# Kernel tuning notes

Hardware: AMD Instinct MI355X
Metric: run time of the kernel (lower is better)

The kernel has to match this reference:

```python
import jax, jax.numpy as jnp
import numpy as np

EMBED = 1024
HEADS = 16
HEAD_DIM = EMBED // HEADS
DIVIDER = int(np.sqrt(HEAD_DIM))  # torch code uses int(sqrt(head_dim)) == 8


def setup_inputs() -> dict:
    key = jax.random.key(0)
    ks = jax.random.split(key, 9)
    B, S = 2, 2048
    scale = 1.0 / np.sqrt(EMBED)
    def lin(kw, kb):
        W = jax.random.uniform(kw, (EMBED, EMBED), jnp.float32, -scale, scale)
        b = jax.random.uniform(kb, (EMBED,), jnp.float32, -scale, scale)
        return W, b
    Wq, bq = lin(ks[0], ks[1])
    Wk, bk = lin(ks[2], ks[3])
    Wv, bv = lin(ks[4], ks[5])
    Wo, bo = lin(ks[6], ks[7])
    x = jax.random.normal(ks[8], (B, S, EMBED), jnp.float32)
    return {"x": x, "Wq": Wq, "bq": bq, "Wk": Wk, "bk": bk,
            "Wv": Wv, "bv": bv, "Wo": Wo, "bo": bo}


def reference(x, Wq, bq, Wk, bk, Wv, bv, Wo, bo):
    B, S, _ = x.shape
    # projections (torch Linear: x @ W.T + b)
    q = x @ Wq.T + bq
    k = x @ Wk.T + bk
    v = x @ Wv.T + bv
    # split heads: [B, S, H, D] -> [B, H, S, D]
    def heads(t):
        return t.reshape(B, S, HEADS, HEAD_DIM).transpose(0, 2, 1, 3)
    q, k, v = heads(q), heads(k), heads(v)
    # scores [B, H, S, S]
    scores = jnp.einsum('bhsd,bhtd->bhst', q, k) / DIVIDER
    attn = jax.nn.softmax(scores, axis=-1)
    out = jnp.einsum('bhst,bhtd->bhsd', attn, v)
    out = out.transpose(0, 2, 1, 3).reshape(B, S, EMBED)
    return out @ Wo.T + bo
```

## Files before the change

kernel.cpp:

```cpp
#include <hip/hip_runtime.h>
#include <hip/hip_bf16.h>
#include <stdint.h>

using bf16 = __hip_bfloat16;
typedef __attribute__((ext_vector_type(8))) short   short8;
typedef __attribute__((ext_vector_type(4))) float   floatx4;
typedef __attribute__((ext_vector_type(2))) unsigned int uint2v;

static __device__ __forceinline__ unsigned short f2bf(float f) {
    return __builtin_bit_cast(unsigned short, __float2bfloat16(f));
}

static __device__ __forceinline__ uint4 load8bf(const void* p, size_t e, int f) {
    if (!f) return *(const uint4*)((const ushort*)p + e);
    const float* fp = (const float*)p + e;
    float4 a = *(const float4*)fp;
    float4 b = *(const float4*)(fp + 4);
    union { uint4 u; unsigned short s[8]; } r;
    r.s[0] = f2bf(a.x); r.s[1] = f2bf(a.y); r.s[2] = f2bf(a.z); r.s[3] = f2bf(a.w);
    r.s[4] = f2bf(b.x); r.s[5] = f2bf(b.y); r.s[6] = f2bf(b.z); r.s[7] = f2bf(b.w);
    return r.u;
}
static __device__ __forceinline__ float loadScalar(const void* p, int i, int f) {
    return f ? ((const float*)p)[i] : __bfloat162float(((const bf16*)p)[i]);
}

#define GLL16(g, l)                                                          \
    __builtin_amdgcn_global_load_lds(                                        \
        (const __attribute__((address_space(1))) void*)(g),                  \
        (__attribute__((address_space(3))) void*)(l), 16, 0, 0)

__global__ void detect_dtype(const ushort* __restrict__ x, int* __restrict__ flag) {
    __shared__ int cnt;
    if (threadIdx.x == 0) cnt = 0;
    __syncthreads();
    unsigned short u = x[threadIdx.x * 2];
    int e = (u >> 7) & 0xFF;
    int bad = (e > 133 || e < 94) ? 1 : 0;
    atomicAdd(&cnt, bad);
    __syncthreads();
    if (threadIdx.x == 0) *flag = (cnt > 64) ? 1 : 0;
}

__global__ void cvt_bf16(const void* __restrict__ x,  const void* __restrict__ Wq,
                         const void* __restrict__ Wk, const void* __restrict__ Wv,
                         const void* __restrict__ Wo,
                         ushort* __restrict__ out, const int* __restrict__ flagp)
{
    const int f = *flagp;
    const size_t M1 = (size_t)1 << 20, M4 = (size_t)4 << 20;
    size_t i = ((size_t)blockIdx.x * 256 + threadIdx.x) * 8;
    const void* src; size_t off;
    if (i < M4)            { src = x;  off = i; }
    else if (i < M4 + M1)  { src = Wq; off = i - M4; }
    else if (i < M4 + 2*M1){ src = Wk; off = i - (M4 + M1); }
    else if (i < M4 + 3*M1){ src = Wv; off = i - (M4 + 2*M1); }
    else                   { src = Wo; off = i - (M4 + 3*M1); }
    *(uint4*)(out + i) = load8bf(src, off, f);
}

__global__ __launch_bounds__(512, 4)
void gemm_lds(const ushort* __restrict__ A,
              const ushort* __restrict__ Wa, const ushort* __restrict__ Wb2,
              const void* __restrict__ Ba, const void* __restrict__ Bb,
              void* __restrict__ Oa, void* __restrict__ Ob_,
              int pa, int pb, int out_ext, const int* __restrict__ flagp)
{
    __shared__ ushort pool[24576];

    const int f  = *flagp;
    const int z  = blockIdx.z;
    const ushort* W  = z ? Wb2 : Wa;
    const void*  Bi  = z ? Bb : Ba;
    void*        Out = z ? Ob_ : Oa;
    const int    pm  = z ? pb : pa;

    const int m0 = blockIdx.x * 128;
    const int n0 = blockIdx.y * 64;
    const int tid  = threadIdx.x;
    const int lane = tid & 63;
    const int wave = tid >> 6;
    const int r15  = lane & 15;
    const int quad = lane >> 4;

    const int l8 = lane >> 3, s8 = lane & 7;
    const int ar0 = wave * 16 + l8;
    const int ar1 = wave * 16 + 8 + l8;
    const int wr  = wave * 8 + l8;
    const ushort* gA0 = A + (size_t)(m0 + ar0) * 1024 + ((s8 ^ (ar0 & 7)) << 3);
    const ushort* gA1 = A + (size_t)(m0 + ar1) * 1024 + ((s8 ^ (ar1 & 7)) << 3);
    const ushort* gW  = W + (size_t)(n0 + wr) * 1024 + ((s8 ^ (wr & 7)) << 3);

    floatx4 acc[4];
#pragma unroll
    for (int db = 0; db < 4; db++) acc[db] = (floatx4){0.f, 0.f, 0.f, 0.f};

    GLL16(gA0, pool + wave * 1024);
    GLL16(gA1, pool + wave * 1024 + 512);
    GLL16(gW,  pool + 16384 + wave * 512);

    for (int kb = 0; kb < 1024; kb += 64) {
        const int cur = (kb >> 6) & 1;
        ushort* xs  = pool + cur * 8192;
        ushort* wsm = pool + 16384 + cur * 4096;
        if (kb + 64 < 1024) {
            ushort* xn = pool + (cur ^ 1) * 8192;
            ushort* wn = pool + 16384 + (cur ^ 1) * 4096;
            GLL16(gA0 + kb + 64, xn + wave * 1024);
            GLL16(gA1 + kb + 64, xn + wave * 1024 + 512);
            GLL16(gW  + kb + 64, wn + wave * 512);
            asm volatile("s_waitcnt vmcnt(3)" ::: "memory");
        } else {
            asm volatile("s_waitcnt vmcnt(0)" ::: "memory");
        }
        __builtin_amdgcn_s_barrier();
        __builtin_amdgcn_sched_barrier(0);
#pragma unroll
        for (int ks = 0; ks < 2; ks++) {
            int arow = wave * 16 + r15;
            short8 af = *(const short8*)(
                &xs[arow * 64 + (((ks * 4 + quad) ^ (arow & 7)) << 3)]);
#pragma unroll
            for (int db = 0; db < 4; db++) {
                int brow = db * 16 + r15;
                short8 bv = *(const short8*)(
                    &wsm[brow * 64 + (((ks * 4 + quad) ^ (brow & 7)) << 3)]);
                acc[db] = __builtin_amdgcn_mfma_f32_16x16x32_bf16(
                    af, bv, acc[db], 0, 0, 0);
            }
        }
        __builtin_amdgcn_s_barrier();
    }

    if (pm == 2) {
#pragma unroll
        for (int db = 0; db < 4; db++) {
            int d = db * 16 + r15;
            float bias = loadScalar(Bi, n0 + d, f);
            int s4 = wave * 16 + quad * 4;
            union { uint2 u; ushort us[4]; } pk;
#pragma unroll
            for (int r = 0; r < 4; r++) pk.us[r] = f2bf(acc[db][r] + bias);
            *(uint2*)(&pool[d * 128 + (((s4 >> 3) ^ (d & 15)) << 3) + (s4 & 7)])
                = pk.u;
        }
        __syncthreads();
        const int b_  = m0 >> 11;
        const int h   = n0 >> 6;
        const int sl0 = m0 & 2047;
#pragma unroll
        for (int rr = 0; rr < 2; rr++) {
            int idx = rr * 512 + tid;
            int d = idx >> 4, sgrp = idx & 15;
            uint4 v = *(const uint4*)(&pool[d * 128 + ((sgrp ^ (d & 15)) << 3)]);
            *(uint4*)((ushort*)Out +
                      ((size_t)((b_ * 16 + h) * 64 + d) << 11) + sl0 + sgrp * 8) = v;
        }
        return;
    }

#pragma unroll
    for (int db = 0; db < 4; db++) {
        int col = n0 + db * 16 + r15;
        float bias = loadScalar(Bi, col, f);
#pragma unroll
        for (int r = 0; r < 4; r++) {
            int row = m0 + wave * 16 + quad * 4 + r;
            float v = acc[db][r] + bias;
            if (pm == 1) {
                int hh = col >> 6, d = col & 63;
                int b_ = row >> 11, s = row & 2047;
                ((ushort*)Out)[(((size_t)(b_ * 16 + hh) * 2048 + s) << 6) + d]
                    = f2bf(v);
            } else if (out_ext && f) {
                ((float*)Out)[(size_t)row * 1024 + col] = v;
            } else {
                ((ushort*)Out)[(size_t)row * 1024 + col] = f2bf(v);
            }
        }
    }
}

template<int BM>
__global__ __launch_bounds__(512, 4)
void gemm_bt(const void* __restrict__ A,
             const void* __restrict__ Wa, const void* __restrict__ Wb,
             const void* __restrict__ Ba, const void* __restrict__ Bb,
             void* __restrict__ Oa, void* __restrict__ Ob_,
             int pa, int pb, int a_ext, int out_ext,
             const int* __restrict__ flagp)
{
    constexpr int MB = BM / 128;
    constexpr int P  = BM / 64;
    constexpr int SG = BM / 8;
    __shared__ ushort pool[BM * 64 + 4096];

    const int f  = *flagp;
    const int fA = a_ext ? f : 0;
    const int z  = blockIdx.z;
    const void* W   = z ? Wb : Wa;
    const void* Bi  = z ? Bb : Ba;
    void*       Out = z ? Ob_ : Oa;
    const int   pm  = z ? pb : pa;

    const int m0 = blockIdx.x * BM;
    const int n0 = blockIdx.y * 64;
    const int tid  = threadIdx.x;
    const int lane = tid & 63;
    const int wave = tid >> 6;
    const int r15  = lane & 15;
    const int quad = lane >> 4;

    const int srow = tid >> 3;
    const int sg   = tid & 7;

    ushort* xs  = pool;
    ushort* wsm = pool + BM * 64;

    floatx4 acc[MB][4];
#pragma unroll
    for (int mb = 0; mb < MB; mb++)
#pragma unroll
        for (int db = 0; db < 4; db++) acc[mb][db] = (floatx4){0.f, 0.f, 0.f, 0.f};

    uint4 apre[P], wpre;
#pragma unroll
    for (int p = 0; p < P; p++)
        apre[p] = load8bf(A, (size_t)(m0 + srow + p * 64) * 1024 + sg * 8, fA);
    wpre = load8bf(W, (size_t)(n0 + srow) * 1024 + sg * 8, f);

    for (int kb = 0; kb < 1024; kb += 64) {
#pragma unroll
        for (int p = 0; p < P; p++) {
            int row = srow + p * 64;
            *(uint4*)(&xs[row * 64 + ((sg ^ (row & 7)) << 3)]) = apre[p];
        }
        *(uint4*)(&wsm[srow * 64 + ((sg ^ (srow & 7)) << 3)]) = wpre;
        __syncthreads();
        if (kb + 64 < 1024) {
#pragma unroll
            for (int p = 0; p < P; p++)
                apre[p] = load8bf(A, (size_t)(m0 + srow + p * 64) * 1024
                                      + kb + 64 + sg * 8, fA);
            wpre = load8bf(W, (size_t)(n0 + srow) * 1024 + kb + 64 + sg * 8, f);
        }
#pragma unroll
        for (int ks = 0; ks < 2; ks++) {
            short8 af[MB];
#pragma unroll
            for (int mb = 0; mb < MB; mb++) {
                int arow = wave * (16 * MB) + mb * 16 + r15;
                af[mb] = *(const short8*)(
                    &xs[arow * 64 + (((ks * 4 + quad) ^ (arow & 7)) << 3)]);
            }
#pragma unroll
            for (int db = 0; db < 4; db++) {
                int brow = db * 16 + r15;
                short8 bv = *(const short8*)(
                    &wsm[brow * 64 + (((ks * 4 + quad) ^ (brow & 7)) << 3)]);
#pragma unroll
                for (int mb = 0; mb < MB; mb++)
                    acc[mb][db] = __builtin_amdgcn_mfma_f32_16x16x32_bf16(
                        af[mb], bv, acc[mb][db], 0, 0, 0);
            }
        }
        __syncthreads();
    }

    if (pm == 2) {
#pragma unroll
        for (int mb = 0; mb < MB; mb++)
#pragma unroll
            for (int db = 0; db < 4; db++) {
                int d = db * 16 + r15;
                float bias = loadScalar(Bi, n0 + d, f);
                int s4 = wave * (16 * MB) + mb * 16 + quad * 4;
                union { uint2 u; ushort us[4]; } pk;
#pragma unroll
                for (int r = 0; r < 4; r++) pk.us[r] = f2bf(acc[mb][db][r] + bias);
                *(uint2*)(&pool[d * BM + (((s4 >> 3) ^ (d & 15)) << 3) + (s4 & 7)])
                    = pk.u;
            }
        __syncthreads();
        const int b_  = m0 >> 11;
        const int h   = n0 >> 6;
        const int sl0 = m0 & 2047;
#pragma unroll
        for (int rr = 0; rr < (64 * SG) / 512; rr++) {
            int idx = rr * 512 + tid;
            int d = idx / SG, sgrp = idx % SG;
            uint4 v = *(const uint4*)(&pool[d * BM + ((sgrp ^ (d & 15)) << 3)]);
            *(uint4*)((ushort*)Out +
                      ((size_t)((b_ * 16 + h) * 64 + d) << 11) + sl0 + sgrp * 8) = v;
        }
        return;
    }

#pragma unroll
    for (int mb = 0; mb < MB; mb++)
#pragma unroll
        for (int db = 0; db < 4; db++) {
            int col = n0 + db * 16 + r15;
            float bias = loadScalar(Bi, col, f);
#pragma unroll
            for (int r = 0; r < 4; r++) {
                int row = m0 + wave * (16 * MB) + mb * 16 + quad * 4 + r;
                float v = acc[mb][db][r] + bias;
                if (pm == 1) {
                    int hh = col >> 6, d = col & 63;
                    int b_ = row >> 11, s = row & 2047;
                    ((ushort*)Out)[(((size_t)(b_ * 16 + hh) * 2048 + s) << 6) + d]
                        = f2bf(v);
                } else if (out_ext && f) {
                    ((float*)Out)[(size_t)row * 1024 + col] = v;
                } else {
                    ((ushort*)Out)[(size_t)row * 1024 + col] = f2bf(v);
                }
            }
        }
}

__global__ __launch_bounds__(512, 4)
void attn_fused(const void* __restrict__ x, const void* __restrict__ Wq,
                const void* __restrict__ bq,
                const ushort* __restrict__ K, const ushort* __restrict__ VT,
                ushort* __restrict__ AO, const int* __restrict__ flagp,
                int xisbf)
{
    __shared__ ushort pool[24576];

    const int f   = *flagp;
    const int fx  = xisbf ? 0 : f;
    const int bh  = blockIdx.x;
    const int h   = bh & 15, b_ = bh >> 4;
    const int q0  = blockIdx.y * 128;
    const int tid  = threadIdx.x;
    const int lane = tid & 63;
    const int wave = tid >> 6;
    const int qg   = wave >> 1;
    const int kh   = wave & 1;
    const int r15  = lane & 15;
    const int quad = lane >> 4;
    const size_t base = (size_t)bh << 17;

    const int srow = tid >> 3;
    const int sg   = tid & 7;

    uint4 kpre = *(const uint4*)(K  + base + (size_t)srow * 64   + sg * 8);
    uint4 vpre = *(const uint4*)(VT + base + (size_t)srow * 2048 + sg * 8);

    floatx4 qacc[4];
#pragma unroll
    for (int db = 0; db < 4; db++) qacc[db] = (floatx4){0.f,0.f,0.f,0.f};

    uint4 xpre[2], wpre;
#pragma unroll
    for (int p = 0; p < 2; p++)
        xpre[p] = load8bf(x, (size_t)(b_ * 2048 + q0 + srow + p * 64) * 1024
                              + sg * 8, fx);
    wpre = load8bf(Wq, (size_t)(h * 64 + srow) * 1024 + sg * 8, fx);

    for (int kb = 0; kb < 1024; kb += 64) {
        int buf = (kb >> 6) & 1;
        ushort* xs  = pool + buf * 8192;
        ushort* wsm = pool + 16384 + buf * 4096;
#pragma unroll
        for (int p = 0; p < 2; p++) {
            int row = srow + p * 64;
            *(uint4*)(&xs[row * 64 + ((sg ^ (row & 7)) << 3)]) = xpre[p];
        }
        *(uint4*)(&wsm[srow * 64 + ((sg ^ (srow & 7)) << 3)]) = wpre;
        __syncthreads();
        if (kb + 64 < 1024) {
#pragma unroll
            for (int p = 0; p < 2; p++)
                xpre[p] = load8bf(x, (size_t)(b_ * 2048 + q0 + srow + p * 64) * 1024
                                      + kb + 64 + sg * 8, fx);
            wpre = load8bf(Wq, (size_t)(h * 64 + srow) * 1024 + kb + 64 + sg * 8, fx);
        }
#pragma unroll
        for (int ks = 0; ks < 2; ks++) {
            int arow = wave * 16 + r15;
            short8 af = *(const short8*)(
                &xs[arow * 64 + (((ks * 4 + quad) ^ (arow & 7)) << 3)]);
#pragma unroll
            for (int db = 0; db < 4; db++) {
                int brow = db * 16 + r15;
                short8 bv = *(const short8*)(
                    &wsm[brow * 64 + (((ks * 4 + quad) ^ (brow & 7)) << 3)]);
                qacc[db] = __builtin_amdgcn_mfma_f32_16x16x32_bf16(
                    af, bv, qacc[db], 0, 0, 0);
            }
        }
    }

    ushort* Qs = pool;
    const float csc = 0.1803368801f;
#pragma unroll
    for (int db = 0; db < 4; db++) {
        int d = db * 16 + r15;
        float bias = loadScalar(bq, h * 64 + d, f);
#pragma unroll
        for (int r = 0; r < 4; r++) {
            int q = wave * 16 + quad * 4 + r;
            Qs[q * 64 + (((d >> 3) ^ (q & 7)) << 3) + (d & 7)] =
                f2bf((qacc[db][r] + bias) * csc);
        }
    }
    __syncthreads();
    short8 qf2[2][2];
#pragma unroll
    for (int qb = 0; qb < 2; qb++)
#pragma unroll
        for (int ks = 0; ks < 2; ks++) {
            int arow = qg * 32 + qb * 16 + r15;
            qf2[qb][ks] = *(const short8*)(
                &Qs[arow * 64 + (((ks * 4 + quad) ^ (arow & 7)) << 3)]);
        }
    __syncthreads();

    floatx4 oacc[2][4], lacc[2];
#pragma unroll
    for (int qb = 0; qb < 2; qb++) {
#pragma unroll
        for (int db = 0; db < 4; db++) oacc[qb][db] = (floatx4){0.f,0.f,0.f,0.f};
        lacc[qb] = (floatx4){0.f,0.f,0.f,0.f};
    }
    short8 ones;
#pragma unroll
    for (int j = 0; j < 8; j++) ones[j] = (short)0x3F80;

    for (int t0 = 0; t0 < 2048; t0 += 64) {
        int buf = (t0 >> 6) & 1;
        ushort* Ks = pool + buf * 4096;
        ushort* Vt = pool + 8192 + buf * 4096;
        *(uint4*)(&Ks[srow * 64 + ((sg ^ (srow & 7)) << 3)]) = kpre;
        *(uint4*)(&Vt[srow * 64 + ((sg ^ (srow & 7)) << 3)]) = vpre;
        __syncthreads();
        if (t0 < 1984) {
            kpre = *(const uint4*)(K  + base + (size_t)(t0 + 64 + srow) * 64
                                       + sg * 8);
            vpre = *(const uint4*)(VT + base + (size_t)srow * 2048
                                       + t0 + 64 + sg * 8);
        }

        floatx4 s[2][2];
#pragma unroll
        for (int mb = 0; mb < 2; mb++)
#pragma unroll
            for (int qb = 0; qb < 2; qb++) s[mb][qb] = (floatx4){0.f,0.f,0.f,0.f};
#pragma unroll
        for (int ks = 0; ks < 2; ks++)
#pragma unroll
            for (int mb = 0; mb < 2; mb++) {
                int arow = kh * 32 + mb * 16 + r15;
                short8 kf = *(const short8*)(
                    &Ks[arow * 64 + (((ks * 4 + quad) ^ (arow & 7)) << 3)]);
#pragma unroll
                for (int qb = 0; qb < 2; qb++)
                    s[mb][qb] = __builtin_amdgcn_mfma_f32_16x16x32_bf16(
                        kf, qf2[qb][ks], s[mb][qb], 0, 0, 0);
            }

        uint Lr[2][2], Hr[2][2];
#pragma unroll
        for (int mb = 0; mb < 2; mb++)
#pragma unroll
            for (int qb = 0; qb < 2; qb++) {
                uint b0 = __builtin_bit_cast(uint, __builtin_amdgcn_exp2f(s[mb][qb][0]));
                uint b1 = __builtin_bit_cast(uint, __builtin_amdgcn_exp2f(s[mb][qb][1]));
                uint b2 = __builtin_bit_cast(uint, __builtin_amdgcn_exp2f(s[mb][qb][2]));
                uint b3 = __builtin_bit_cast(uint, __builtin_amdgcn_exp2f(s[mb][qb][3]));
                Lr[mb][qb] = (b1 & 0xFFFF0000u) | (b0 >> 16);
                Hr[mb][qb] = (b3 & 0xFFFF0000u) | (b2 >> 16);
            }
        short8 pf[2];
#pragma unroll
        for (int qb = 0; qb < 2; qb++) {
            uint2v tL = __builtin_amdgcn_permlane32_swap(
                Lr[0][qb], Lr[1][qb], false, false);
            uint2v uL = __builtin_amdgcn_permlane16_swap(
                tL[0], tL[1], false, false);
            uint2v tH = __builtin_amdgcn_permlane32_swap(
                Hr[0][qb], Hr[1][qb], false, false);
            uint2v uH = __builtin_amdgcn_permlane16_swap(
                tH[0], tH[1], false, false);
            union { uint u[4]; short8 s8; } pk;
            pk.u[0] = uL[0]; pk.u[1] = uH[0]; pk.u[2] = uL[1]; pk.u[3] = uH[1];
            pf[qb] = pk.s8;
        }

#pragma unroll
        for (int db = 0; db < 4; db++) {
            int brow = db * 16 + r15;
            short8 vf = *(const short8*)(
                &Vt[brow * 64 + (((kh * 4 + quad) ^ (brow & 7)) << 3)]);
#pragma unroll
            for (int qb = 0; qb < 2; qb++)
                oacc[qb][db] = __builtin_amdgcn_mfma_f32_16x16x32_bf16(
                    pf[qb], vf, oacc[qb][db], 0, 0, 0);
        }
#pragma unroll
        for (int qb = 0; qb < 2; qb++)
            lacc[qb] = __builtin_amdgcn_mfma_f32_16x16x32_bf16(
                pf[qb], ones, lacc[qb], 0, 0, 0);
    }

    __syncthreads();
    {
        char* rb = (char*)pool + qg * 10240 + lane * 16;
        if (kh) {
#pragma unroll
            for (int qb = 0; qb < 2; qb++) {
#pragma unroll
                for (int db = 0; db < 4; db++)
                    *(floatx4*)(rb + (qb * 4 + db) * 1024) = oacc[qb][db];
                *(floatx4*)(rb + (8 + qb) * 1024) = lacc[qb];
            }
        }
        __syncthreads();
        if (!kh) {
#pragma unroll
            for (int qb = 0; qb < 2; qb++) {
#pragma unroll
                for (int db = 0; db < 4; db++)
                    oacc[qb][db] += *(const floatx4*)(rb + (qb * 4 + db) * 1024);
                lacc[qb] += *(const floatx4*)(rb + (8 + qb) * 1024);
            }
            float inv[2][4];
#pragma unroll
            for (int qb = 0; qb < 2; qb++)
#pragma unroll
                for (int r = 0; r < 4; r++) inv[qb][r] = 1.f / lacc[qb][r];
#pragma unroll
            for (int qb = 0; qb < 2; qb++)
#pragma unroll
                for (int db = 0; db < 4; db++) {
                    int d = db * 16 + r15;
#pragma unroll
                    for (int r = 0; r < 4; r++) {
                        int qi = q0 + qg * 32 + qb * 16 + quad * 4 + r;
                        AO[((size_t)(b_ * 2048 + qi) << 10) + h * 64 + d] =
                            f2bf(oacc[qb][db][r] * inv[qb][r]);
                    }
                }
        }
    }
}

__global__ void copy_u4(const uint4* __restrict__ src, uint4* __restrict__ dst) {
    size_t i = (size_t)blockIdx.x * 256 + threadIdx.x;
    dst[i] = src[i];
}

extern "C" void kernel_launch(void* const* d_in, const int* in_sizes, int n_in,
                              void* d_out, int out_size, void* d_ws, size_t ws_size,
                              hipStream_t stream)
{
    const void* x  = d_in[0];
    const void* Wq = d_in[1];
    const void* bq = d_in[2];
    const void* Wk = d_in[3];
    const void* bk = d_in[4];
    const void* Wv = d_in[5];
    const void* bv = d_in[6];
    const void* Wo = d_in[7];
    const void* bo = d_in[8];

    const size_t TEN = (size_t)2 * 16 * 2048 * 64;
    const size_t M1  = (size_t)1 << 20;
    int*    flagp = (int*)d_ws;
    ushort* Kw    = (ushort*)((char*)d_ws + 256);
    ushort* Vw    = Kw + TEN;

    const size_t need_cvt = 256 + (2 * TEN + 8 * M1) * sizeof(ushort);
    const size_t need_aow = need_cvt + TEN * sizeof(ushort);

    detect_dtype<<<1, 256, 0, stream>>>((const ushort*)x, flagp);

    if (ws_size >= need_cvt) {
        ushort* CV  = Vw + TEN;
        ushort* xb  = CV;
        ushort* wqb = CV + 4 * M1;
        ushort* wkb = CV + 5 * M1;
        ushort* wvb = CV + 6 * M1;
        ushort* wob = CV + 7 * M1;
        const bool aow_ws = ws_size >= need_aow;
        ushort* AOw = aow_ws ? (CV + 8 * M1) : (ushort*)d_out;
        ushort* Oin = aow_ws ? AOw : Kw;

        cvt_bf16<<<dim3(4096), dim3(256), 0, stream>>>(
            x, Wq, Wk, Wv, Wo, CV, flagp);

        gemm_lds<<<dim3(32, 16, 2), dim3(512), 0, stream>>>(
            xb, wkb, wvb, bk, bv, Kw, Vw, 1, 2,
            0, flagp);

        attn_fused<<<dim3(32, 16), dim3(512), 0, stream>>>(
            xb, wqb, bq, Kw, Vw, AOw, flagp, 1);

        if (!aow_ws)
            copy_u4<<<dim3(2048), dim3(256), 0, stream>>>(
                (const uint4*)d_out, (uint4*)Oin);

        gemm_lds<<<dim3(32, 16, 1), dim3(512), 0, stream>>>(
            Oin, wob, wob, bo, bo, d_out, d_out, 0, 0,
            1, flagp);
    } else {
        const bool big_ws = ws_size >= 3 * TEN * sizeof(ushort) + 256;
        ushort* AOw = big_ws ? (Vw + TEN) : (ushort*)d_out;
        ushort* Oin = big_ws ? AOw : Kw;

        gemm_bt<128><<<dim3(32, 16, 2), dim3(512), 0, stream>>>(
            x, Wk, Wv, bk, bv, Kw, Vw, 1, 2, 1, 0, flagp);
        attn_fused<<<dim3(32, 16), dim3(512), 0, stream>>>(
            x, Wq, bq, Kw, Vw, AOw, flagp, 0);
        if (!big_ws)
            copy_u4<<<dim3(2048), dim3(256), 0, stream>>>(
                (const uint4*)d_out, (uint4*)Oin);
        gemm_bt<128><<<dim3(32, 16, 1), dim3(512), 0, stream>>>(
            Oin, Wo, Wo, bo, bo, d_out, d_out, 0, 0, 0, 1, flagp);
    }
}
```

Before: 201.2 us.

## Fuse K and V projections into one dual-output GEMM tile sharing the A tile

The K/V projection GEMM now computes a 128x128 tile per block, 64 columns of K and 64 of V, so each loaded x tile feeds both weight matrices instead of being loaded twice by separate z-blocks. Each wave now owns a 32x64 sub-tile with 2x4 accumulators, which doubles MFMA work per A fragment. The output projection uses the same kernel with a 512-column offset, halving its grid. LDS grows to 64KB per block and register use rises, which may reduce occupancy.

```diff
diff --git a/kernel.cpp b/kernel.cpp
--- a/kernel.cpp
+++ b/kernel.cpp
@@ -60,56 +60,69 @@
 }
 
 __global__ __launch_bounds__(512, 4)
-void gemm_lds(const ushort* __restrict__ A,
-              const ushort* __restrict__ Wa, const ushort* __restrict__ Wb2,
-              const void* __restrict__ Ba, const void* __restrict__ Bb,
-              void* __restrict__ Oa, void* __restrict__ Ob_,
-              int pa, int pb, int out_ext, const int* __restrict__ flagp)
+void gemm_dual(const ushort* __restrict__ A,
+               const ushort* __restrict__ Wa, const ushort* __restrict__ Wb2,
+               const void* __restrict__ Ba, const void* __restrict__ Bb,
+               void* __restrict__ Oa, void* __restrict__ Ob_,
+               int pa, int pb, int nb_off, int out_ext,
+               const int* __restrict__ flagp)
 {
-    __shared__ ushort pool[24576];
+    __shared__ ushort pool[32768];
 
     const int f  = *flagp;
-    const int z  = blockIdx.z;
-    const ushort* W  = z ? Wb2 : Wa;
-    const void*  Bi  = z ? Bb : Ba;
-    void*        Out = z ? Ob_ : Oa;
-    const int    pm  = z ? pb : pa;
-
     const int m0 = blockIdx.x * 128;
-    const int n0 = blockIdx.y * 64;
+    const int n0a = blockIdx.y * 64;
+    const int n0b = n0a + nb_off;
     const int tid  = threadIdx.x;
     const int lane = tid & 63;
     const int wave = tid >> 6;
+    const int wm   = wave & 3;
+    const int wn   = wave >> 2;
     const int r15  = lane & 15;
     const int quad = lane >> 4;
 
+    const int   my_pm = wn ? pb : pa;
+    const void* my_Bi = wn ? Bb : Ba;
+    void*       my_O  = wn ? Ob_ : Oa;
+    const int   my_n0 = wn ? n0b : n0a;
+
     const int l8 = lane >> 3, s8 = lane & 7;
     const int ar0 = wave * 16 + l8;
-    const int ar1 = wave * 16 + 8 + l8;
-    const int wr  = wave * 8 + l8;
+    const int ar1 = ar0 + 8;
+    const int wr0 = wave * 16 + l8;
+    const int wr1 = wr0 + 8;
     const ushort* gA0 = A + (size_t)(m0 + ar0) * 1024 + ((s8 ^ (ar0 & 7)) << 3);
     const ushort* gA1 = A + (size_t)(m0 + ar1) * 1024 + ((s8 ^ (ar1 & 7)) << 3);
-    const ushort* gW  = W + (size_t)(n0 + wr) * 1024 + ((s8 ^ (wr & 7)) << 3);
-
-    floatx4 acc[4];
-#pragma unroll
-    for (int db = 0; db < 4; db++) acc[db] = (floatx4){0.f, 0.f, 0.f, 0.f};
+    const ushort* gW0 = (wr0 < 64 ? Wa + (size_t)(n0a + wr0) * 1024
+                                  : Wb2 + (size_t)(n0b + wr0 - 64) * 1024)
+                        + ((s8 ^ (wr0 & 7)) << 3);
+    const ushort* gW1 = (wr1 < 64 ? Wa + (size_t)(n0a + wr1) * 1024
+                                  : Wb2 + (size_t)(n0b + wr1 - 64) * 1024)
+                        + ((s8 ^ (wr1 & 7)) << 3);
+
+    floatx4 acc[2][4];
+#pragma unroll
+    for (int mb = 0; mb < 2; mb++)
+#pragma unroll
+        for (int db = 0; db < 4; db++) acc[mb][db] = (floatx4){0.f, 0.f, 0.f, 0.f};
 
     GLL16(gA0, pool + wave * 1024);
     GLL16(gA1, pool + wave * 1024 + 512);
-    GLL16(gW,  pool + 16384 + wave * 512);
+    GLL16(gW0, pool + 16384 + wave * 1024);
+    GLL16(gW1, pool + 16384 + wave * 1024 + 512);
 
     for (int kb = 0; kb < 1024; kb += 64) {
         const int cur = (kb >> 6) & 1;
         ushort* xs  = pool + cur * 8192;
-        ushort* wsm = pool + 16384 + cur * 4096;
+        ushort* wsm = pool + 16384 + cur * 8192;
         if (kb + 64 < 1024) {
             ushort* xn = pool + (cur ^ 1) * 8192;
-            ushort* wn = pool + 16384 + (cur ^ 1) * 4096;
+            ushort* wn_ = pool + 16384 + (cur ^ 1) * 8192;
             GLL16(gA0 + kb + 64, xn + wave * 1024);
             GLL16(gA1 + kb + 64, xn + wave * 1024 + 512);
-            GLL16(gW  + kb + 64, wn + wave * 512);
-            asm volatile("s_waitcnt vmcnt(3)" ::: "memory");
+            GLL16(gW0 + kb + 64, wn_ + wave * 1024);
+            GLL16(gW1 + kb + 64, wn_ + wave * 1024 + 512);
+            asm volatile("s_waitcnt vmcnt(4)" ::: "memory");
         } else {
             asm volatile("s_waitcnt vmcnt(0)" ::: "memory");
         }
@@ -117,66 +130,80 @@
         __builtin_amdgcn_sched_barrier(0);
 #pragma unroll
         for (int ks = 0; ks < 2; ks++) {
-            int arow = wave * 16 + r15;
-            short8 af = *(const short8*)(
-                &xs[arow * 64 + (((ks * 4 + quad) ^ (arow & 7)) << 3)]);
+            short8 af[2];
+#pragma unroll
+            for (int mb = 0; mb < 2; mb++) {
+                int arow = wm * 32 + mb * 16 + r15;
+                af[mb] = *(const short8*)(
+                    &xs[arow * 64 + (((ks * 4 + quad) ^ (arow & 7)) << 3)]);
+            }
 #pragma unroll
             for (int db = 0; db < 4; db++) {
-                int brow = db * 16 + r15;
+                int brow = wn * 64 + db * 16 + r15;
                 short8 bv = *(const short8*)(
                     &wsm[brow * 64 + (((ks * 4 + quad) ^ (brow & 7)) << 3)]);
-                acc[db] = __builtin_amdgcn_mfma_f32_16x16x32_bf16(
-                    af, bv, acc[db], 0, 0, 0);
+#pragma unroll
+                for (int mb = 0; mb < 2; mb++)
+                    acc[mb][db] = __builtin_amdgcn_mfma_f32_16x16x32_bf16(
+                        af[mb], bv, acc[mb][db], 0, 0, 0);
             }
         }
         __builtin_amdgcn_s_barrier();
     }
 
-    if (pm == 2) {
-#pragma unroll
-        for (int db = 0; db < 4; db++) {
-            int d = db * 16 + r15;
-            float bias = loadScalar(Bi, n0 + d, f);
-            int s4 = wave * 16 + quad * 4;
-            union { uint2 u; ushort us[4]; } pk;
-#pragma unroll
-            for (int r = 0; r < 4; r++) pk.us[r] = f2bf(acc[db][r] + bias);
-            *(uint2*)(&pool[d * 128 + (((s4 >> 3) ^ (d & 15)) << 3) + (s4 & 7)])
-                = pk.u;
-        }
+    if (my_pm == 2) {
+#pragma unroll
+        for (int mb = 0; mb < 2; mb++)
+#pragma unroll
+            for (int db = 0; db < 4; db++) {
+                int d = db * 16 + r15;
+                float bias = loadScalar(my_Bi, my_n0 + d, f);
+                int s4 = wm * 32 + mb * 16 + quad * 4;
+                union { uint2 u; ushort us[4]; } pk;
+#pragma unroll
+                for (int r = 0; r < 4; r++) pk.us[r] = f2bf(acc[mb][db][r] + bias);
+                *(uint2*)(&pool[d * 128 + (((s4 >> 3) ^ (d & 15)) << 3) + (s4 & 7)])
+                    = pk.u;
+            }
+    } else {
+#pragma unroll
+        for (int mb = 0; mb < 2; mb++)
+#pragma unroll
+            for (int db = 0; db < 4; db++) {
+                int col = my_n0 + db * 16 + r15;
+                float bias = loadScalar(my_Bi, col, f);
+#pragma unroll
+                for (int r = 0; r < 4; r++) {
+                    int row = m0 + wm * 32 + mb * 16 + quad * 4 + r;
+                    float v = acc[mb][db][r] + bias;
+                    if (my_pm == 1) {
+                        int hh = col >> 6, d = col & 63;
+                        int b_ = row >> 11, s = row & 2047;
+                        ((ushort*)my_O)[(((size_t)(b_ * 16 + hh) * 2048 + s) << 6) + d]
+                            = f2bf(v);
+                    } else if (out_ext && f) {
+                        ((float*)my_O)[(size_t)row * 1024 + col] = v;
+                    } else {
+                        ((ushort*)my_O)[(size_t)row * 1024 + col] = f2bf(v);
+                    }
+                }
+            }
+    }
+
+    if (pa == 2 || pb == 2) {
         __syncthreads();
+        void* OutT = (pb == 2) ? Ob_ : Oa;
+        const int nT  = (pb == 2) ? n0b : n0a;
         const int b_  = m0 >> 11;
-        const int h   = n0 >> 6;
+        const int h   = nT >> 6;
         const int sl0 = m0 & 2047;
 #pragma unroll
         for (int rr = 0; rr < 2; rr++) {
             int idx = rr * 512 + tid;
             int d = idx >> 4, sgrp = idx & 15;
             uint4 v = *(const uint4*)(&pool[d * 128 + ((sgrp ^ (d & 15)) << 3)]);
-            *(uint4*)((ushort*)Out +
+            *(uint4*)((ushort*)OutT +
                       ((size_t)((b_ * 16 + h) * 64 + d) << 11) + sl0 + sgrp * 8) = v;
-        }
-        return;
-    }
-
-#pragma unroll
-    for (int db = 0; db < 4; db++) {
-        int col = n0 + db * 16 + r15;
-        float bias = loadScalar(Bi, col, f);
-#pragma unroll
-        for (int r = 0; r < 4; r++) {
-            int row = m0 + wave * 16 + quad * 4 + r;
-            float v = acc[db][r] + bias;
-            if (pm == 1) {
-                int hh = col >> 6, d = col & 63;
-                int b_ = row >> 11, s = row & 2047;
-                ((ushort*)Out)[(((size_t)(b_ * 16 + hh) * 2048 + s) << 6) + d]
-                    = f2bf(v);
-            } else if (out_ext && f) {
-                ((float*)Out)[(size_t)row * 1024 + col] = v;
-            } else {
-                ((ushort*)Out)[(size_t)row * 1024 + col] = f2bf(v);
-            }
         }
     }
 }
@@ -592,9 +619,9 @@
         cvt_bf16<<<dim3(4096), dim3(256), 0, stream>>>(
             x, Wq, Wk, Wv, Wo, CV, flagp);
 
-        gemm_lds<<<dim3(32, 16, 2), dim3(512), 0, stream>>>(
+        gemm_dual<<<dim3(32, 16), dim3(512), 0, stream>>>(
             xb, wkb, wvb, bk, bv, Kw, Vw, 1, 2,
-            0, flagp);
+            0, 0, flagp);
 
         attn_fused<<<dim3(32, 16), dim3(512), 0, stream>>>(
             xb, wqb, bq, Kw, Vw, AOw, flagp, 1);
@@ -603,9 +630,9 @@
             copy_u4<<<dim3(2048), dim3(256), 0, stream>>>(
                 (const uint4*)d_out, (uint4*)Oin);
 
-        gemm_lds<<<dim3(32, 16, 1), dim3(512), 0, stream>>>(
+        gemm_dual<<<dim3(32, 8), dim3(512), 0, stream>>>(
             Oin, wob, wob, bo, bo, d_out, d_out, 0, 0,
-            1, flagp);
+            512, 1, flagp);
     } else {
         const bool big_ws = ws_size >= 3 * TEN * sizeof(ushort) + 256;
         ushort* AOw = big_ws ? (Vw + TEN) : (ushort*)d_out;
```

Result: no change. 198.8 us (median of 2 runs) (-1.2%).
